# Kernel optimization log

Measured on AMD Instinct MI355X. Metric: run time of the kernel, lower is better.

The kernel has to match this reference:

```python
import jax, jax.numpy as jnp
import numpy as np

N_NODES = 100000


def gcn_conv(x, edge_index, W, b):
    """PyG GCNConv: symmetric normalization with added self-loops.
    x: [N, Fin], edge_index: [2, E], W: [Fin, Fout], b: [Fout]
    """
    n = x.shape[0]
    h = x @ W  # [N, Fout] dense transform first (standard GCNConv order)
    loops = jnp.arange(n, dtype=edge_index.dtype)
    src = jnp.concatenate([edge_index[0], loops])  # self-loops appended
    dst = jnp.concatenate([edge_index[1], loops])
    deg = jax.ops.segment_sum(jnp.ones_like(dst, dtype=h.dtype), dst, num_segments=n)
    dinv = jax.lax.rsqrt(deg)  # deg >= 1 thanks to self-loops
    norm = dinv[src] * dinv[dst]  # [E+N]
    msgs = h[src] * norm[:, None]  # gather + scale
    out = jax.ops.segment_sum(msgs, dst, num_segments=n)  # scatter-add
    return out + b


def setup_inputs() -> dict:
    key = jax.random.key(0)
    k = jax.random.split(key, 9)
    in_c, hid, out_c = 128, 128, 64
    n_edges = 1600000
    x = jax.random.normal(k[0], (N_NODES, in_c), dtype=jnp.float32)
    edge_index = jax.random.randint(k[1], (2, n_edges), 0, N_NODES, dtype=jnp.int64)
    def lin(kw, kb, fan_in, fan_out):
        bound = 1.0 / np.sqrt(fan_in)
        W = jax.random.uniform(kw, (fan_in, fan_out), jnp.float32, -bound, bound)
        b = jax.random.uniform(kb, (fan_out,), jnp.float32, -bound, bound)
        return W, b
    W1, b1 = lin(k[2], k[3], in_c, hid)
    W2, b2 = lin(k[4], k[5], hid, hid)
    Wf, bf = lin(k[6], k[7], hid, out_c)
    return {"x": x, "edge_index": edge_index, "W1": W1, "b1": b1,
            "W2": W2, "b2": b2, "Wf": Wf, "bf": bf}


def reference(x, edge_index, W1, b1, W2, b2, Wf, bf):
    h = jax.nn.relu(gcn_conv(x, edge_index, W1, b1))
    h = jax.nn.relu(gcn_conv(h, edge_index, W2, b2))
    return h @ Wf + bf
```

## Files before the change

kernel.cpp:

```cpp
#include <hip/hip_runtime.h>
#include <stdint.h>

typedef short short8 __attribute__((ext_vector_type(8)));
typedef float floatx4 __attribute__((ext_vector_type(4)));

#define BK 256

static __device__ __forceinline__ float bflo(unsigned int u) {
    union { unsigned int i; float f; } v; v.i = u << 16; return v.f;
}
static __device__ __forceinline__ float bfhi(unsigned int u) {
    union { unsigned int i; float f; } v; v.i = u & 0xffff0000u; return v.f;
}
static __device__ __forceinline__ unsigned short f2bf(float f) {
    union { float f; unsigned int i; } v; v.f = f;
    unsigned int u = v.i;
    unsigned int r = u + 0x7fffu + ((u >> 16) & 1u);
    return (unsigned short)(r >> 16);
}


__global__ void k_zero_cnt(int* bucket_cnt, int K) {
    int i = blockIdx.x * 256 + threadIdx.x;
    if (i < K) bucket_cnt[i] = 0;
}

__global__ __launch_bounds__(256) void k_hist(const int* __restrict__ dst, int* bucket_cnt,
                                              int E, int N, int K) {
    __shared__ int h[4][512];
    int t = threadIdx.x, w = t >> 6;
    for (int i = t; i < 4 * 512; i += 256) ((int*)h)[i] = 0;
    __syncthreads();
    int per = (E + gridDim.x - 1) / gridDim.x;
    int lo = blockIdx.x * per, hi = min(lo + per, E);
    for (int e = lo + t; e < hi; e += 256) {
        unsigned int d = (unsigned int)dst[e];
        if (d < (unsigned int)N) atomicAdd(&h[w][d >> 8], 1);
    }
    __syncthreads();
    for (int i = t; i < K; i += 256) {
        int c = h[0][i] + h[1][i] + h[2][i] + h[3][i];
        if (c) atomicAdd(&bucket_cnt[i], c);
    }
}

__global__ void k_scanK(const int* __restrict__ bucket_cnt, int* bucket_off, int* bucket_cur,
                        int* row_start, int K, int N) {
    __shared__ int s[512];
    int t = threadIdx.x;
    int v = (t < K) ? bucket_cnt[t] : 0;
    s[t] = v; __syncthreads();
    for (int off = 1; off < 512; off <<= 1) {
        int x = (t >= off) ? s[t - off] : 0;
        __syncthreads();
        s[t] += x;
        __syncthreads();
    }
    if (t < K) { bucket_off[t] = s[t] - v; bucket_cur[t] = s[t] - v; }
    if (t == K - 1) { bucket_off[K] = s[t]; row_start[N] = s[t]; }
}

__global__ __launch_bounds__(256) void k_binscatter(const int* __restrict__ src,
                                                    const int* __restrict__ dst,
                                                    int* bucket_cur, unsigned int* __restrict__ tmp,
                                                    int E, int N, int K) {
    __shared__ int h[4][512];
    int t = threadIdx.x, w = t >> 6;
    for (int i = t; i < 4 * 512; i += 256) ((int*)h)[i] = 0;
    __syncthreads();
    int per = (E + gridDim.x - 1) / gridDim.x;
    int lo = blockIdx.x * per, hi = min(lo + per, E);
    for (int e = lo + t; e < hi; e += 256) {
        unsigned int d = (unsigned int)dst[e];
        if (d < (unsigned int)N) atomicAdd(&h[w][d >> 8], 1);
    }
    __syncthreads();
    for (int k = t; k < K; k += 256) {
        int c0 = h[0][k], c1 = h[1][k], c2 = h[2][k], c3 = h[3][k];
        int tot = c0 + c1 + c2 + c3;
        int base = tot ? atomicAdd(&bucket_cur[k], tot) : 0;
        h[0][k] = base; h[1][k] = base + c0; h[2][k] = base + c0 + c1;
        h[3][k] = base + c0 + c1 + c2;
    }
    __syncthreads();
    for (int e = lo + t; e < hi; e += 256) {
        unsigned int d = (unsigned int)dst[e];
        if (d < (unsigned int)N) {
            unsigned int sv = (unsigned int)src[e];
            if (sv >= (unsigned int)N) sv = 0;
            int p = atomicAdd(&h[w][d >> 8], 1);
            tmp[p] = (sv << 8) | (d & 255u);
        }
    }
}

__global__ __launch_bounds__(256) void k_fine(const unsigned int* __restrict__ tmp,
                                              const int* __restrict__ bucket_off,
                                              int* __restrict__ row_start, float* __restrict__ dinv,
                                              int* __restrict__ csr, int N) {
    __shared__ int deg4[4][BK];
    __shared__ int scn[BK];
    __shared__ int cur[BK];
    int b = blockIdx.x, t = threadIdx.x, w = t >> 6;
    int lo = bucket_off[b], hi = bucket_off[b + 1];
    for (int i = t; i < 4 * BK; i += 256) ((int*)deg4)[i] = 0;
    __syncthreads();
    for (int e = lo + t; e < hi; e += 256) atomicAdd(&deg4[w][tmp[e] & 255u], 1);
    __syncthreads();
    int v = deg4[0][t] + deg4[1][t] + deg4[2][t] + deg4[3][t];
    scn[t] = v; __syncthreads();
    for (int off = 1; off < 256; off <<= 1) {
        int x = (t >= off) ? scn[t - off] : 0;
        __syncthreads();
        scn[t] += x;
        __syncthreads();
    }
    int rs = lo + scn[t] - v;
    cur[t] = rs;
    int node = b * BK + t;
    if (node < N) { row_start[node] = rs; dinv[node] = rsqrtf((float)(v + 1)); }
    __syncthreads();
    for (int e = lo + t; e < hi; e += 256) {
        unsigned int p = tmp[e];
        int pos = atomicAdd(&cur[p & 255u], 1);
        csr[pos] = (int)(p >> 8);
    }
}


__global__ void k_wconv_all(const float* __restrict__ W1, const float* __restrict__ W2,
                            const float* __restrict__ Wf, unsigned short* __restrict__ wb1,
                            unsigned short* __restrict__ wb2, unsigned short* __restrict__ wbf) {
    int i = blockIdx.x * 256 + threadIdx.x;
    if (i < 16384) {
        int k = i >> 7, n = i & 127;
        wb1[n * 128 + k] = f2bf(W1[i]);
    } else if (i < 32768) {
        int j = i - 16384, k = j >> 7, n = j & 127;
        wb2[n * 128 + k] = f2bf(W2[j]);
    } else if (i < 40960) {
        int j = i - 32768, k = j >> 6, n = j & 63;
        wbf[n * 128 + k] = f2bf(Wf[j]);
    }
}


template <int NOUT, bool SCALE, bool BIAS, bool XF32, bool OUTF32>
__global__ __launch_bounds__(256, 2) void k_gemm(
    const void* __restrict__ Xv, const unsigned short* __restrict__ Wbf,
    const float* __restrict__ bias, const float* __restrict__ dinv,
    void* __restrict__ outv, int M, int MB) {
    __shared__ __align__(16) unsigned short Wl[NOUT * 136];
    int t = threadIdx.x;
    for (int c = t; c < NOUT * 16; c += 256) {
        short8 v = *(const short8*)(Wbf + (size_t)c * 8);
        *(short8*)(&Wl[(c >> 4) * 136 + (c & 15) * 8]) = v;
    }
    __syncthreads();

    int wave = t >> 6, lane = t & 63;
    int quad = lane >> 4, l16 = lane & 15;
    constexpr int NT = NOUT / 16;

    for (int mb = blockIdx.x; mb < MB; mb += gridDim.x) {
        int m0 = mb * 64 + wave * 16;
        int mr = m0 + l16;
        int mrc = mr < M ? mr : M - 1;

        floatx4 acc[NT];
#pragma unroll
        for (int i = 0; i < NT; i++) acc[i] = (floatx4){0.f, 0.f, 0.f, 0.f};

#pragma unroll
        for (int kc = 0; kc < 4; kc++) {
            short8 a;
            if (XF32) {
                const float* X = (const float*)Xv;
                const float* p = X + (size_t)mrc * 128 + kc * 32 + quad * 8;
                float4 xa = *(const float4*)p;
                float4 xb = *(const float4*)(p + 4);
                a[0] = (short)f2bf(xa.x); a[1] = (short)f2bf(xa.y);
                a[2] = (short)f2bf(xa.z); a[3] = (short)f2bf(xa.w);
                a[4] = (short)f2bf(xb.x); a[5] = (short)f2bf(xb.y);
                a[6] = (short)f2bf(xb.z); a[7] = (short)f2bf(xb.w);
            } else {
                const unsigned short* X = (const unsigned short*)Xv;
                a = *(const short8*)(X + (size_t)mrc * 128 + kc * 32 + quad * 8);
            }
#pragma unroll
            for (int nt = 0; nt < NT; nt++) {
                short8 b = *(const short8*)(&Wl[(nt * 16 + l16) * 136 + kc * 32 + quad * 8]);
                acc[nt] = __builtin_amdgcn_mfma_f32_16x16x32_bf16(a, b, acc[nt], 0, 0, 0);
            }
        }

#pragma unroll
        for (int i = 0; i < 4; i++) {
            int r = m0 + quad * 4 + i;
            if (r >= M) continue;
            float sc = SCALE ? dinv[r] : 1.0f;
#pragma unroll
            for (int nt = 0; nt < NT; nt++) {
                int n = nt * 16 + l16;
                float v = acc[nt][i] * sc;
                if (BIAS) v += bias[n];
                if (OUTF32) {
                    ((float*)outv)[(size_t)r * NOUT + n] = v;
                } else {
                    ((unsigned short*)outv)[(size_t)r * NOUT + n] = f2bf(v);
                }
            }
        }
    }
}


__global__ __launch_bounds__(256, 8) void k_aggregate(
    const unsigned short* __restrict__ Hs, const int* __restrict__ csr,
    const int* __restrict__ row_start,
    const float* __restrict__ dinv, const float* __restrict__ bias,
    unsigned short* __restrict__ out, int N, int E) {
    int wave = threadIdx.x >> 6, lane = threadIdx.x & 63;
    int grp = lane >> 4, c16 = lane & 15;
    int node = blockIdx.x * 4 + wave;
    if (node >= N) return;
    int Nm1 = N - 1;
    int cb = c16 * 8;

    float a0 = 0.f, a1 = 0.f, a2 = 0.f, a3 = 0.f, a4 = 0.f, a5 = 0.f, a6 = 0.f, a7 = 0.f;

    int start = row_start[node];
    int end = row_start[node + 1];
    if (start < 0) start = 0;
    if (end > E) end = E;
    int cnt = end - start;
    int full4 = cnt >> 2;

    int it = 0;
    for (; it + 2 <= full4; it += 2) {
        int eA = start + it * 4 + grp;
        int eB = eA + 4;
        int iA = min(max(csr[eA], 0), Nm1);
        int iB = min(max(csr[eB], 0), Nm1);
        uint4 uA = *(const uint4*)(Hs + (size_t)iA * 128 + cb);
        uint4 uB = *(const uint4*)(Hs + (size_t)iB * 128 + cb);
        a0 += bflo(uA.x); a1 += bfhi(uA.x); a2 += bflo(uA.y); a3 += bfhi(uA.y);
        a4 += bflo(uA.z); a5 += bfhi(uA.z); a6 += bflo(uA.w); a7 += bfhi(uA.w);
        a0 += bflo(uB.x); a1 += bfhi(uB.x); a2 += bflo(uB.y); a3 += bfhi(uB.y);
        a4 += bflo(uB.z); a5 += bfhi(uB.z); a6 += bflo(uB.w); a7 += bfhi(uB.w);
    }
    for (; it < full4; it++) {
        int eA = start + it * 4 + grp;
        int iA = min(max(csr[eA], 0), Nm1);
        uint4 uA = *(const uint4*)(Hs + (size_t)iA * 128 + cb);
        a0 += bflo(uA.x); a1 += bfhi(uA.x); a2 += bflo(uA.y); a3 += bfhi(uA.y);
        a4 += bflo(uA.z); a5 += bfhi(uA.z); a6 += bflo(uA.w); a7 += bfhi(uA.w);
    }
    int eT = start + full4 * 4 + grp;
    if (eT < end) {
        int iT = min(max(csr[eT], 0), Nm1);
        uint4 uT = *(const uint4*)(Hs + (size_t)iT * 128 + cb);
        a0 += bflo(uT.x); a1 += bfhi(uT.x); a2 += bflo(uT.y); a3 += bfhi(uT.y);
        a4 += bflo(uT.z); a5 += bfhi(uT.z); a6 += bflo(uT.w); a7 += bfhi(uT.w);
    }

    a0 += __shfl_xor(a0, 16); a1 += __shfl_xor(a1, 16); a2 += __shfl_xor(a2, 16);
    a3 += __shfl_xor(a3, 16); a4 += __shfl_xor(a4, 16); a5 += __shfl_xor(a5, 16);
    a6 += __shfl_xor(a6, 16); a7 += __shfl_xor(a7, 16);
    a0 += __shfl_xor(a0, 32); a1 += __shfl_xor(a1, 32); a2 += __shfl_xor(a2, 32);
    a3 += __shfl_xor(a3, 32); a4 += __shfl_xor(a4, 32); a5 += __shfl_xor(a5, 32);
    a6 += __shfl_xor(a6, 32); a7 += __shfl_xor(a7, 32);

    uint4 us = *(const uint4*)(Hs + (size_t)node * 128 + cb);
    a0 += bflo(us.x); a1 += bfhi(us.x); a2 += bflo(us.y); a3 += bfhi(us.y);
    a4 += bflo(us.z); a5 += bfhi(us.z); a6 += bflo(us.w); a7 += bfhi(us.w);

    float di = dinv[node];
    float4 b0 = *(const float4*)(bias + cb);
    float4 b1 = *(const float4*)(bias + cb + 4);
    float r0 = fmaxf(fmaf(di, a0, b0.x), 0.f);
    float r1 = fmaxf(fmaf(di, a1, b0.y), 0.f);
    float r2 = fmaxf(fmaf(di, a2, b0.z), 0.f);
    float r3 = fmaxf(fmaf(di, a3, b0.w), 0.f);
    float r4 = fmaxf(fmaf(di, a4, b1.x), 0.f);
    float r5 = fmaxf(fmaf(di, a5, b1.y), 0.f);
    float r6 = fmaxf(fmaf(di, a6, b1.z), 0.f);
    float r7 = fmaxf(fmaf(di, a7, b1.w), 0.f);
    if (grp == 0) {
        uint4 o;
        o.x = (unsigned int)f2bf(r0) | ((unsigned int)f2bf(r1) << 16);
        o.y = (unsigned int)f2bf(r2) | ((unsigned int)f2bf(r3) << 16);
        o.z = (unsigned int)f2bf(r4) | ((unsigned int)f2bf(r5) << 16);
        o.w = (unsigned int)f2bf(r6) | ((unsigned int)f2bf(r7) << 16);
        *(uint4*)(out + (size_t)node * 128 + cb) = o;
    }
}


extern "C" void kernel_launch(void* const* d_in, const int* in_sizes, int n_in,
                              void* d_out, int out_size, void* d_ws, size_t ws_size,
                              hipStream_t stream) {
    const float* x  = (const float*)d_in[0];
    const int* ei   = (const int*)d_in[1];
    const float* W1 = (const float*)d_in[2];
    const float* b1 = (const float*)d_in[3];
    const float* W2 = (const float*)d_in[4];
    const float* b2 = (const float*)d_in[5];
    const float* Wf = (const float*)d_in[6];
    const float* bf = (const float*)d_in[7];

    int N = in_sizes[0] / 128;
    int E = in_sizes[1] / 2;
    const int* src = ei;
    const int* dst = ei + E;
    int K = (N + BK - 1) / BK;
    if (N >= (1 << 24) || K > 512) return;

    size_t need = 0;
    auto pad = [](size_t b) { return (b + 255) & ~(size_t)255; };
    size_t o_bcnt = need; need += pad(512 * 4);
    size_t o_boff = need; need += pad(513 * 4);
    size_t o_bcur = need; need += pad(512 * 4);
    size_t o_rs   = need; need += pad(((size_t)N + 1) * 4);
    size_t o_dinv = need; need += pad((size_t)N * 4);
    size_t o_wbf  = need; need += pad((16384 + 16384 + 8192) * 2);
    size_t o_csr  = need; need += pad((size_t)E * 4);
    size_t o_hs   = need; need += pad((size_t)N * 128 * 2);
    size_t o_a    = need; need += pad((size_t)N * 128 * 2);
    if (ws_size < need) return;
    if ((size_t)E * 4 > (size_t)N * 128 * 2) return;

    char* ws = (char*)d_ws;
    int* bucket_cnt = (int*)(ws + o_bcnt);
    int* bucket_off = (int*)(ws + o_boff);
    int* bucket_cur = (int*)(ws + o_bcur);
    int* row_start  = (int*)(ws + o_rs);
    float* dinv     = (float*)(ws + o_dinv);
    unsigned short* wb1 = (unsigned short*)(ws + o_wbf);
    unsigned short* wb2 = wb1 + 16384;
    unsigned short* wbf = wb2 + 16384;
    int* csr        = (int*)(ws + o_csr);
    unsigned short* Hs = (unsigned short*)(ws + o_hs);
    unsigned short* A  = (unsigned short*)(ws + o_a);
    unsigned int* tmp  = (unsigned int*)A;

    k_wconv_all<<<160, 256, 0, stream>>>(W1, W2, Wf, wb1, wb2, wbf);

    k_zero_cnt<<<2, 256, 0, stream>>>(bucket_cnt, 512);
    k_hist<<<256, 256, 0, stream>>>(dst, bucket_cnt, E, N, K);
    k_scanK<<<1, 512, 0, stream>>>(bucket_cnt, bucket_off, bucket_cur, row_start, K, N);
    k_binscatter<<<256, 256, 0, stream>>>(src, dst, bucket_cur, tmp, E, N, K);
    k_fine<<<K, 256, 0, stream>>>(tmp, bucket_off, row_start, dinv, csr, N);

    int MB = (N + 63) / 64;
    int GG = (MB + 1) / 2;

    k_gemm<128, true, false, true, false><<<GG, 256, 0, stream>>>(x, wb1, nullptr, dinv, Hs, N, MB);
    k_aggregate<<<(N + 3) / 4, 256, 0, stream>>>(Hs, csr, row_start, dinv, b1, A, N, E);
    k_gemm<128, true, false, false, false><<<GG, 256, 0, stream>>>(A, wb2, nullptr, dinv, Hs, N, MB);
    k_aggregate<<<(N + 3) / 4, 256, 0, stream>>>(Hs, csr, row_start, dinv, b2, A, N, E);
    k_gemm<64, false, true, false, true><<<GG, 256, 0, stream>>>(A, wbf, bf, nullptr, d_out, N, MB);
}
```

Measured before the change: 340.8 us.

## Merge weight conversion with histogram, deepen aggregate unroll, nontemporal csr/out access

Merges the weight bf16 conversion kernel and the destination histogram kernel into one launch, removing a kernel launch. The aggregation loop is unrolled to four outstanding neighbour row gathers per lane, with nontemporal loads for the CSR index stream and a nontemporal store for the output. GEMM launch bounds are raised to 3 or 4 waves per SIMD minimum, which may force register spills.

```diff
diff --git a/kernel.cpp b/kernel.cpp
--- a/kernel.cpp
+++ b/kernel.cpp
@@ -3,6 +3,7 @@
 
 typedef short short8 __attribute__((ext_vector_type(8)));
 typedef float floatx4 __attribute__((ext_vector_type(4)));
+typedef unsigned int uintx4 __attribute__((ext_vector_type(4)));
 
 #define BK 256
 
@@ -20,28 +21,50 @@
 }
 
 
+#define HB 256
+
+__global__ __launch_bounds__(256) void k_prep(
+    const float* __restrict__ W1, const float* __restrict__ W2, const float* __restrict__ Wf,
+    unsigned short* __restrict__ wb1, unsigned short* __restrict__ wb2,
+    unsigned short* __restrict__ wbf, int* bucket_cnt,
+    const int* __restrict__ dst, int E, int N, int K) {
+    int blk = blockIdx.x;
+    int t = threadIdx.x;
+    if (blk < 160) {
+        int i = blk * 256 + t;
+        if (i < 16384) {
+            int k = i >> 7, n = i & 127;
+            wb1[n * 128 + k] = f2bf(W1[i]);
+        } else if (i < 32768) {
+            int j = i - 16384, k = j >> 7, n = j & 127;
+            wb2[n * 128 + k] = f2bf(W2[j]);
+        } else if (i < 40960) {
+            int j = i - 32768, k = j >> 6, n = j & 63;
+            wbf[n * 128 + k] = f2bf(Wf[j]);
+        }
+        return;
+    }
+    __shared__ int h[4][512];
+    int w = t >> 6;
+    for (int i = t; i < 4 * 512; i += 256) ((int*)h)[i] = 0;
+    __syncthreads();
+    int hb = blk - 160;
+    int per = (E + HB - 1) / HB;
+    int lo = hb * per, hi = min(lo + per, E);
+    for (int e = lo + t; e < hi; e += 256) {
+        unsigned int d = (unsigned int)dst[e];
+        if (d < (unsigned int)N) atomicAdd(&h[w][d >> 8], 1);
+    }
+    __syncthreads();
+    for (int i = t; i < K; i += 256) {
+        int c = h[0][i] + h[1][i] + h[2][i] + h[3][i];
+        if (c) atomicAdd(&bucket_cnt[i], c);
+    }
+}
+
 __global__ void k_zero_cnt(int* bucket_cnt, int K) {
     int i = blockIdx.x * 256 + threadIdx.x;
     if (i < K) bucket_cnt[i] = 0;
-}
-
-__global__ __launch_bounds__(256) void k_hist(const int* __restrict__ dst, int* bucket_cnt,
-                                              int E, int N, int K) {
-    __shared__ int h[4][512];
-    int t = threadIdx.x, w = t >> 6;
-    for (int i = t; i < 4 * 512; i += 256) ((int*)h)[i] = 0;
-    __syncthreads();
-    int per = (E + gridDim.x - 1) / gridDim.x;
-    int lo = blockIdx.x * per, hi = min(lo + per, E);
-    for (int e = lo + t; e < hi; e += 256) {
-        unsigned int d = (unsigned int)dst[e];
-        if (d < (unsigned int)N) atomicAdd(&h[w][d >> 8], 1);
-    }
-    __syncthreads();
-    for (int i = t; i < K; i += 256) {
-        int c = h[0][i] + h[1][i] + h[2][i] + h[3][i];
-        if (c) atomicAdd(&bucket_cnt[i], c);
-    }
 }
 
 __global__ void k_scanK(const int* __restrict__ bucket_cnt, int* bucket_off, int* bucket_cur,
@@ -128,25 +151,8 @@
 }
 
 
-__global__ void k_wconv_all(const float* __restrict__ W1, const float* __restrict__ W2,
-                            const float* __restrict__ Wf, unsigned short* __restrict__ wb1,
-                            unsigned short* __restrict__ wb2, unsigned short* __restrict__ wbf) {
-    int i = blockIdx.x * 256 + threadIdx.x;
-    if (i < 16384) {
-        int k = i >> 7, n = i & 127;
-        wb1[n * 128 + k] = f2bf(W1[i]);
-    } else if (i < 32768) {
-        int j = i - 16384, k = j >> 7, n = j & 127;
-        wb2[n * 128 + k] = f2bf(W2[j]);
-    } else if (i < 40960) {
-        int j = i - 32768, k = j >> 6, n = j & 63;
-        wbf[n * 128 + k] = f2bf(Wf[j]);
-    }
-}
-
-
-template <int NOUT, bool SCALE, bool BIAS, bool XF32, bool OUTF32>
-__global__ __launch_bounds__(256, 2) void k_gemm(
+template <int NOUT, bool SCALE, bool BIAS, bool XF32, bool OUTF32, int MINW>
+__global__ __launch_bounds__(256, MINW) void k_gemm(
     const void* __restrict__ Xv, const unsigned short* __restrict__ Wbf,
     const float* __restrict__ bias, const float* __restrict__ dinv,
     void* __restrict__ outv, int M, int MB) {
@@ -237,29 +243,36 @@
     int full4 = cnt >> 2;
 
     int it = 0;
-    for (; it + 2 <= full4; it += 2) {
+    for (; it + 4 <= full4; it += 4) {
+        int e0 = start + it * 4 + grp;
+        int i0 = min(max(__builtin_nontemporal_load(csr + e0), 0), Nm1);
+        int i1 = min(max(__builtin_nontemporal_load(csr + e0 + 4), 0), Nm1);
+        int i2 = min(max(__builtin_nontemporal_load(csr + e0 + 8), 0), Nm1);
+        int i3 = min(max(__builtin_nontemporal_load(csr + e0 + 12), 0), Nm1);
+        uintx4 u0 = *(const uintx4*)(Hs + (size_t)i0 * 128 + cb);
+        uintx4 u1 = *(const uintx4*)(Hs + (size_t)i1 * 128 + cb);
+        uintx4 u2 = *(const uintx4*)(Hs + (size_t)i2 * 128 + cb);
+        uintx4 u3 = *(const uintx4*)(Hs + (size_t)i3 * 128 + cb);
+        a0 += bflo(u0.x); a1 += bfhi(u0.x); a2 += bflo(u0.y); a3 += bfhi(u0.y);
+        a4 += bflo(u0.z); a5 += bfhi(u0.z); a6 += bflo(u0.w); a7 += bfhi(u0.w);
+        a0 += bflo(u1.x); a1 += bfhi(u1.x); a2 += bflo(u1.y); a3 += bfhi(u1.y);
+        a4 += bflo(u1.z); a5 += bfhi(u1.z); a6 += bflo(u1.w); a7 += bfhi(u1.w);
+        a0 += bflo(u2.x); a1 += bfhi(u2.x); a2 += bflo(u2.y); a3 += bfhi(u2.y);
+        a4 += bflo(u2.z); a5 += bfhi(u2.z); a6 += bflo(u2.w); a7 += bfhi(u2.w);
+        a0 += bflo(u3.x); a1 += bfhi(u3.x); a2 += bflo(u3.y); a3 += bfhi(u3.y);
+        a4 += bflo(u3.z); a5 += bfhi(u3.z); a6 += bflo(u3.w); a7 += bfhi(u3.w);
+    }
+    for (; it < full4; it++) {
         int eA = start + it * 4 + grp;
-        int eB = eA + 4;
-        int iA = min(max(csr[eA], 0), Nm1);
-        int iB = min(max(csr[eB], 0), Nm1);
-        uint4 uA = *(const uint4*)(Hs + (size_t)iA * 128 + cb);
-        uint4 uB = *(const uint4*)(Hs + (size_t)iB * 128 + cb);
+        int iA = min(max(__builtin_nontemporal_load(csr + eA), 0), Nm1);
+        uintx4 uA = *(const uintx4*)(Hs + (size_t)iA * 128 + cb);
         a0 += bflo(uA.x); a1 += bfhi(uA.x); a2 += bflo(uA.y); a3 += bfhi(uA.y);
         a4 += bflo(uA.z); a5 += bfhi(uA.z); a6 += bflo(uA.w); a7 += bfhi(uA.w);
-        a0 += bflo(uB.x); a1 += bfhi(uB.x); a2 += bflo(uB.y); a3 += bfhi(uB.y);
-        a4 += bflo(uB.z); a5 += bfhi(uB.z); a6 += bflo(uB.w); a7 += bfhi(uB.w);
-    }
-    for (; it < full4; it++) {
-        int eA = start + it * 4 + grp;
-        int iA = min(max(csr[eA], 0), Nm1);
-        uint4 uA = *(const uint4*)(Hs + (size_t)iA * 128 + cb);
-        a0 += bflo(uA.x); a1 += bfhi(uA.x); a2 += bflo(uA.y); a3 += bfhi(uA.y);
-        a4 += bflo(uA.z); a5 += bfhi(uA.z); a6 += bflo(uA.w); a7 += bfhi(uA.w);
     }
     int eT = start + full4 * 4 + grp;
     if (eT < end) {
-        int iT = min(max(csr[eT], 0), Nm1);
-        uint4 uT = *(const uint4*)(Hs + (size_t)iT * 128 + cb);
+        int iT = min(max(__builtin_nontemporal_load(csr + eT), 0), Nm1);
+        uintx4 uT = *(const uintx4*)(Hs + (size_t)iT * 128 + cb);
         a0 += bflo(uT.x); a1 += bfhi(uT.x); a2 += bflo(uT.y); a3 += bfhi(uT.y);
         a4 += bflo(uT.z); a5 += bfhi(uT.z); a6 += bflo(uT.w); a7 += bfhi(uT.w);
     }
@@ -271,7 +284,7 @@
     a3 += __shfl_xor(a3, 32); a4 += __shfl_xor(a4, 32); a5 += __shfl_xor(a5, 32);
     a6 += __shfl_xor(a6, 32); a7 += __shfl_xor(a7, 32);
 
-    uint4 us = *(const uint4*)(Hs + (size_t)node * 128 + cb);
+    uintx4 us = *(const uintx4*)(Hs + (size_t)node * 128 + cb);
     a0 += bflo(us.x); a1 += bfhi(us.x); a2 += bflo(us.y); a3 += bfhi(us.y);
     a4 += bflo(us.z); a5 += bfhi(us.z); a6 += bflo(us.w); a7 += bfhi(us.w);
 
@@ -287,12 +300,12 @@
     float r6 = fmaxf(fmaf(di, a6, b1.z), 0.f);
     float r7 = fmaxf(fmaf(di, a7, b1.w), 0.f);
     if (grp == 0) {
-        uint4 o;
+        uintx4 o;
         o.x = (unsigned int)f2bf(r0) | ((unsigned int)f2bf(r1) << 16);
         o.y = (unsigned int)f2bf(r2) | ((unsigned int)f2bf(r3) << 16);
         o.z = (unsigned int)f2bf(r4) | ((unsigned int)f2bf(r5) << 16);
         o.w = (unsigned int)f2bf(r6) | ((unsigned int)f2bf(r7) << 16);
-        *(uint4*)(out + (size_t)node * 128 + cb) = o;
+        __builtin_nontemporal_store(o, (uintx4*)(out + (size_t)node * 128 + cb));
     }
 }
 
@@ -344,10 +357,8 @@
     unsigned short* A  = (unsigned short*)(ws + o_a);
     unsigned int* tmp  = (unsigned int*)A;
 
-    k_wconv_all<<<160, 256, 0, stream>>>(W1, W2, Wf, wb1, wb2, wbf);
-
     k_zero_cnt<<<2, 256, 0, stream>>>(bucket_cnt, 512);
-    k_hist<<<256, 256, 0, stream>>>(dst, bucket_cnt, E, N, K);
+    k_prep<<<160 + HB, 256, 0, stream>>>(W1, W2, Wf, wb1, wb2, wbf, bucket_cnt, dst, E, N, K);
     k_scanK<<<1, 512, 0, stream>>>(bucket_cnt, bucket_off, bucket_cur, row_start, K, N);
     k_binscatter<<<256, 256, 0, stream>>>(src, dst, bucket_cur, tmp, E, N, K);
     k_fine<<<K, 256, 0, stream>>>(tmp, bucket_off, row_start, dinv, csr, N);
@@ -355,9 +366,9 @@
     int MB = (N + 63) / 64;
     int GG = (MB + 1) / 2;
 
-    k_gemm<128, true, false, true, false><<<GG, 256, 0, stream>>>(x, wb1, nullptr, dinv, Hs, N, MB);
+    k_gemm<128, true, false, true, false, 3><<<GG, 256, 0, stream>>>(x, wb1, nullptr, dinv, Hs, N, MB);
     k_aggregate<<<(N + 3) / 4, 256, 0, stream>>>(Hs, csr, row_start, dinv, b1, A, N, E);
-    k_gemm<128, true, false, false, false><<<GG, 256, 0, stream>>>(A, wb2, nullptr, dinv, Hs, N, MB);
+    k_gemm<128, true, false, false, false, 3><<<GG, 256, 0, stream>>>(A, wb2, nullptr, dinv, Hs, N, MB);
     k_aggregate<<<(N + 3) / 4, 256, 0, stream>>>(Hs, csr, row_start, dinv, b2, A, N, E);
-    k_gemm<64, false, true, false, true><<<GG, 256, 0, stream>>>(A, wbf, bf, nullptr, d_out, N, MB);
-}
+    k_gemm<64, false, true, false, true, 4><<<GG, 256, 0, stream>>>(A, wbf, bf, nullptr, d_out, N, MB);
+}
```

After: 380.3 us. 11.6% more time.
